# Optimization experiments

Hardware: AMD Instinct MI355X
Metric: run time of the kernel (lower is better)

Reference implementation:

```python
import jax, jax.numpy as jnp
import numpy as np

DIM = 1024
HEADS = 8
DIM_HEAD = 64
INNER = HEADS * DIM_HEAD  # 512


def setup_inputs() -> dict:
    key = jax.random.key(0)
    k1, k2, k3, k4 = jax.random.split(key, 4)
    x = jax.random.normal(k1, (4, 4096, DIM), dtype=jnp.float32)
    W_qkv = jax.random.normal(k2, (DIM, 3 * INNER), dtype=jnp.float32) * (DIM ** -0.5)
    W_out = jax.random.normal(k3, (INNER, DIM), dtype=jnp.float32) * (INNER ** -0.5)
    b_out = jax.random.normal(k4, (DIM,), dtype=jnp.float32) * 0.01
    return {"x": x, "W_qkv": W_qkv, "W_out": W_out, "b_out": b_out}


def reference(x, W_qkv, W_out, b_out):
    b, n, _ = x.shape
    qkv = x @ W_qkv                                   # [b, n, 3*inner]
    q, k, v = jnp.split(qkv, 3, axis=-1)              # each [b, n, inner]

    def to_heads(t):
        return t.reshape(b, n, HEADS, DIM_HEAD).transpose(0, 2, 1, 3)  # [b, h, n, d]

    q = jax.nn.elu(to_heads(q)) + 1.0
    k = jax.nn.elu(to_heads(k)) + 1.0
    v = to_heads(v)
    # kv summary matrix: [b, h, d, e]
    context = jnp.einsum('bhnd,bhne->bhde', k, v)
    out = jnp.einsum('bhde,bhnd->bhne', context, q)   # [b, h, n, e]
    out = out.transpose(0, 2, 1, 3).reshape(b, n, INNER)
    return out @ W_out + b_out
```

## Files before the change

### kernel.cpp

```cpp
#include <hip/hip_runtime.h>
#include <hip/hip_bf16.h>
#include <cstdint>

typedef __attribute__((ext_vector_type(4))) float f32x4;
typedef __attribute__((ext_vector_type(8))) short bf16x8;

__device__ __forceinline__ ushort f2bf(float f) {
  unsigned u = __builtin_bit_cast(unsigned, f);
  u += 0x7fffu + ((u >> 16) & 1u);
  return (ushort)(u >> 16);
}
__device__ __forceinline__ float bf2f(ushort h) {
  unsigned u = ((unsigned)h) << 16;
  return __builtin_bit_cast(float, u);
}

__device__ __forceinline__ void gload_lds16(const ushort* g, ushort* l) {
  __builtin_amdgcn_global_load_lds(
      (const __attribute__((address_space(1))) unsigned int*)g,
      (__attribute__((address_space(3))) unsigned int*)l, 16, 0, 0);
}

__device__ __forceinline__ void hard_barrier() {
  __builtin_amdgcn_sched_barrier(0);
  __builtin_amdgcn_s_barrier();
  __builtin_amdgcn_sched_barrier(0);
}

template <int N>
__device__ __forceinline__ void wait_vm() {
  if constexpr (N == 0) asm volatile("s_waitcnt vmcnt(0)" ::: "memory");
  else if constexpr (N == 4) asm volatile("s_waitcnt vmcnt(4)" ::: "memory");
  else static_assert(N < 0, "unsupported vmcnt");
}

__global__ __launch_bounds__(256) void cvt_x_kernel(const float4* __restrict__ x,
                                                    ushort4* __restrict__ xb, int n4) {
  int stride = gridDim.x * blockDim.x;
  for (int i = blockIdx.x * blockDim.x + threadIdx.x; i < n4; i += stride) {
    float4 f = x[i];
    ushort4 o;
    o.x = f2bf(f.x); o.y = f2bf(f.y); o.z = f2bf(f.z); o.w = f2bf(f.w);
    xb[i] = o;
  }
}

__global__ __launch_bounds__(256) void transpose_w_kernel(const float* __restrict__ W,
                                                          ushort* __restrict__ Wt) {
  __shared__ float tile[32][33];
  int n0 = blockIdx.x * 32;
  int k0 = blockIdx.y * 32;
  int tx = threadIdx.x;
  int ty = threadIdx.y;
  #pragma unroll
  for (int p = 0; p < 4; ++p) {
    int k = k0 + ty + p * 8;
    tile[ty + p * 8][tx] = W[(size_t)k * 1536 + n0 + tx];
  }
  __syncthreads();
  #pragma unroll
  for (int p = 0; p < 4; ++p) {
    int n = n0 + ty + p * 8;
    Wt[(size_t)n * 1024 + k0 + tx] = f2bf(tile[tx][ty + p * 8]);
  }
}

template <int LDA, int LDB, int NT>
__device__ __forceinline__ void gemm_core8(const ushort* __restrict__ A,
                                           const ushort* __restrict__ Bt,
                                           int row0, int col0, f32x4 acc[8][4],
                                           ushort* lds) {
  const int tid = threadIdx.x;
  const int l = tid & 63;
  const int wid = tid >> 6;
  const int fr = l & 15, fq = l >> 4;
  const int wr = wid >> 2, wc = wid & 3;

  const int srow = tid >> 2;
  const int lam = (tid & 3) ^ ((tid >> 3) & 3);
  const ushort* aG = A + (size_t)(row0 + srow) * LDA + lam * 8;
  const ushort* bG = Bt + (size_t)(col0 + srow) * LDB + lam * 8;

  auto stageA = [&](int tt, int kap) {
    ushort* d = lds + (tt & 1) * 32768 + kap * 8192 + tid * 8;
    const ushort* s = aG + tt * 64 + kap * 32;
    gload_lds16(s, d);
    gload_lds16(s + (size_t)128 * LDA, d + 4096);
  };
  auto stageB = [&](int tt, int kap) {
    ushort* d = lds + (tt & 1) * 32768 + 16384 + kap * 8192 + tid * 8;
    const ushort* s = bG + tt * 64 + kap * 32;
    gload_lds16(s, d);
    gload_lds16(s + (size_t)128 * LDB, d + 4096);
  };

  const int sig = fq ^ ((fr >> 1) & 3);
  const int aOff = wr * 4096 + fr * 32 + sig * 8;
  const int bOff = 16384 + wc * 2048 + fr * 32 + sig * 8;

  auto mfma16 = [&](const bf16x8 av[4], const bf16x8 bv[4], int mh) {
    __builtin_amdgcn_s_setprio(1);
    #pragma unroll
    for (int mm = 0; mm < 4; ++mm)
      #pragma unroll
      for (int n = 0; n < 4; ++n)
        acc[mh * 4 + mm][n] =
            __builtin_amdgcn_mfma_f32_16x16x32_bf16(av[mm], bv[n], acc[mh * 4 + mm][n], 0, 0, 0);
    __builtin_amdgcn_s_setprio(0);
  };

  stageA(0, 0); stageB(0, 0); stageA(0, 1); stageB(0, 1);
  wait_vm<4>();
  hard_barrier();

  for (int t = 0; t < NT; ++t) {
    const ushort* sb = lds + (t & 1) * 32768;
    const bool pre = (t + 1 < NT);
    bf16x8 av[4], bv[4];

    #pragma unroll
    for (int mm = 0; mm < 4; ++mm) av[mm] = *(const bf16x8*)(sb + aOff + mm * 512);
    #pragma unroll
    for (int n = 0; n < 4; ++n) bv[n] = *(const bf16x8*)(sb + bOff + n * 512);
    if (pre) stageA(t + 1, 0);
    hard_barrier();
    mfma16(av, bv, 0);

    #pragma unroll
    for (int mm = 0; mm < 4; ++mm) av[mm] = *(const bf16x8*)(sb + aOff + 2048 + mm * 512);
    if (pre) { stageB(t + 1, 0); wait_vm<4>(); } else { wait_vm<0>(); }
    hard_barrier();
    mfma16(av, bv, 1);

    #pragma unroll
    for (int mm = 0; mm < 4; ++mm) av[mm] = *(const bf16x8*)(sb + 8192 + aOff + mm * 512);
    #pragma unroll
    for (int n = 0; n < 4; ++n) bv[n] = *(const bf16x8*)(sb + 8192 + bOff + n * 512);
    if (pre) stageA(t + 1, 1);
    hard_barrier();
    mfma16(av, bv, 0);

    #pragma unroll
    for (int mm = 0; mm < 4; ++mm) av[mm] = *(const bf16x8*)(sb + 8192 + aOff + 2048 + mm * 512);
    if (pre) { stageB(t + 1, 1); wait_vm<4>(); }
    hard_barrier();
    mfma16(av, bv, 1);
  }
}

__device__ __forceinline__ void swz_grid(int nx, int& bx, int& by) {
  const int bid = blockIdx.x;
  const int nwg = gridDim.x;
  const int cpx = nwg >> 3;
  const int swz = (bid & 7) * cpx + (bid >> 3);
  by = swz / nx;
  bx = swz - by * nx;
}

__global__ __launch_bounds__(512, 1) void gemm_qkv_kernel(const ushort* __restrict__ xb,
                                                          const ushort* __restrict__ wt,
                                                          ushort* __restrict__ qkv) {
  __shared__ ushort lds[65536];
  f32x4 acc[8][4] = {};
  int bx, by;
  swz_grid(64, bx, by);
  const int row0 = bx * 256;
  const int col0 = by * 256;
  gemm_core8<1024, 1024, 16>(xb, wt, row0, col0, acc, lds);
  const int l = threadIdx.x & 63;
  const int wid = threadIdx.x >> 6;
  const int wr = wid >> 2, wc = wid & 3;
  const int fr = l & 15, fq = l >> 4;
  #pragma unroll
  for (int m = 0; m < 8; ++m) {
    #pragma unroll
    for (int n = 0; n < 4; ++n) {
      const int c = col0 + wc * 64 + n * 16 + fr;
      #pragma unroll
      for (int j = 0; j < 4; ++j) {
        const int r = row0 + wr * 128 + m * 16 + fq * 4 + j;
        float v = acc[m][n][j];
        if (c < 1024) v = (v > 0.f) ? (v + 1.f) : __expf(v);
        qkv[(size_t)r * 1536 + c] = f2bf(v);
      }
    }
  }
}

__global__ __launch_bounds__(256) void ctx_kernel(const ushort* __restrict__ qkv,
                                                  float* __restrict__ part) {
  const int bh = blockIdx.x;
  const int split = blockIdx.y;
  const int b = bh >> 3, h = bh & 7;
  const int t = threadIdx.x;
  const int d0 = (t >> 4) * 4;
  const int e0 = (t & 15) * 4;
  __shared__ ushort ks[64][64];
  __shared__ ushort vs[64][64];
  float acc[4][4] = {};
  const int rowBase = b * 4096 + split * 256;
  for (int chunk = 0; chunk < 256; chunk += 64) {
    __syncthreads();
    #pragma unroll
    for (int p = 0; p < 2; ++p) {
      const int r = (t >> 3) + p * 32;
      const int c = (t & 7) * 8;
      const ushort* src = qkv + (size_t)(rowBase + chunk + r) * 1536;
      *(uint4*)&ks[r][c] = *(const uint4*)(src + 512 + h * 64 + c);
      *(uint4*)&vs[r][c] = *(const uint4*)(src + 1024 + h * 64 + c);
    }
    __syncthreads();
    for (int r = 0; r < 64; ++r) {
      ushort4 ku = *(const ushort4*)&ks[r][d0];
      ushort4 vu = *(const ushort4*)&vs[r][e0];
      float kk[4] = {bf2f(ku.x), bf2f(ku.y), bf2f(ku.z), bf2f(ku.w)};
      float vv[4] = {bf2f(vu.x), bf2f(vu.y), bf2f(vu.z), bf2f(vu.w)};
      #pragma unroll
      for (int i = 0; i < 4; ++i)
        #pragma unroll
        for (int j = 0; j < 4; ++j)
          acc[i][j] += kk[i] * vv[j];
    }
  }
  float* dst = part + ((size_t)split * 32 + bh) * 4096;
  #pragma unroll
  for (int i = 0; i < 4; ++i)
    #pragma unroll
    for (int j = 0; j < 4; ++j)
      dst[(d0 + i) * 64 + (e0 + j)] = acc[i][j];
}

__global__ __launch_bounds__(256) void ctx_reduce_kernel(const float* __restrict__ part,
                                                         float* __restrict__ ctx) {
  const int i = blockIdx.x * 256 + threadIdx.x;
  float s = 0.f;
  #pragma unroll
  for (int sp = 0; sp < 16; ++sp) s += part[(size_t)sp * 131072 + i];
  ctx[i] = s;
}

__global__ __launch_bounds__(256) void weff_kernel(const float* __restrict__ ctx,
                                                   const float* __restrict__ Wout,
                                                   ushort* __restrict__ weff) {
  const int bh = blockIdx.x;
  const int h = bh & 7;
  const int m0 = blockIdx.y * 128;
  const int t = threadIdx.x;
  __shared__ float cs[64 * 64];
  __shared__ float ws[64][128];
  #pragma unroll
  for (int p = 0; p < 4; ++p) {
    const int idx = p * 1024 + t * 4;
    *(float4*)&cs[idx] = *(const float4*)&ctx[(size_t)bh * 4096 + idx];
  }
  #pragma unroll
  for (int p = 0; p < 8; ++p) {
    const int e = (t >> 5) + p * 8;
    const int c = (t & 31) * 4;
    *(float4*)&ws[e][c] = *(const float4*)&Wout[(size_t)(h * 64 + e) * 1024 + m0 + c];
  }
  __syncthreads();
  const int m = t & 127;
  const int dh = (t >> 7) * 32;
  float acc[32] = {};
  for (int e = 0; e < 64; ++e) {
    const float w = ws[e][m];
    #pragma unroll
    for (int i = 0; i < 32; ++i)
      acc[i] += cs[(dh + i) * 64 + e] * w;
  }
  ushort* dst = weff + ((size_t)(bh >> 3) * 1024 + m0 + m) * 512 + h * 64 + dh;
  #pragma unroll
  for (int i = 0; i < 32; ++i) dst[i] = f2bf(acc[i]);
}

__global__ __launch_bounds__(512, 1) void gemm_out_kernel(const ushort* __restrict__ qkv,
                                                          const ushort* __restrict__ weff,
                                                          const float* __restrict__ bout,
                                                          float* __restrict__ out) {
  __shared__ ushort lds[65536];
  f32x4 acc[8][4] = {};
  int bx, by;
  swz_grid(64, bx, by);
  const int row0 = bx * 256;
  const int col0 = by * 256;
  const int b = row0 >> 12;
  gemm_core8<1536, 512, 8>(qkv, weff + (size_t)b * 1024 * 512, row0, col0, acc, lds);
  const int l = threadIdx.x & 63;
  const int wid = threadIdx.x >> 6;
  const int wr = wid >> 2, wc = wid & 3;
  const int fr = l & 15, fq = l >> 4;
  #pragma unroll
  for (int m = 0; m < 8; ++m) {
    #pragma unroll
    for (int n = 0; n < 4; ++n) {
      const int c = col0 + wc * 64 + n * 16 + fr;
      const float bb = bout[c];
      #pragma unroll
      for (int j = 0; j < 4; ++j) {
        const int r = row0 + wr * 128 + m * 16 + fq * 4 + j;
        out[(size_t)r * 1024 + c] = acc[m][n][j] + bb;
      }
    }
  }
}

extern "C" void kernel_launch(void* const* d_in, const int* in_sizes, int n_in,
                              void* d_out, int out_size, void* d_ws, size_t ws_size,
                              hipStream_t stream) {
  const float* x    = (const float*)d_in[0];
  const float* Wqkv = (const float*)d_in[1];
  const float* Wout = (const float*)d_in[2];
  const float* bout = (const float*)d_in[3];
  float* out = (float*)d_out;
  char* ws = (char*)d_ws;

  ushort* xb   = (ushort*)(ws);
  ushort* wt   = (ushort*)(ws + 33554432);
  ushort* qkv  = (ushort*)(ws + 36700160);
  float*  part = (float* )(ws + 87031808);
  float*  ctx  = (float* )(ws + 95420416);
  ushort* weff = (ushort*)(ws + 95944704);

  cvt_x_kernel<<<2048, 256, 0, stream>>>((const float4*)x, (ushort4*)xb, 16384 * 1024 / 4);
  transpose_w_kernel<<<dim3(48, 32), dim3(32, 8), 0, stream>>>(Wqkv, wt);
  gemm_qkv_kernel<<<384, 512, 0, stream>>>(xb, wt, qkv);
  ctx_kernel<<<dim3(32, 16), 256, 0, stream>>>(qkv, part);
  ctx_reduce_kernel<<<512, 256, 0, stream>>>(part, ctx);
  weff_kernel<<<dim3(32, 8), 256, 0, stream>>>(ctx, Wout, weff);
  gemm_out_kernel<<<256, 512, 0, stream>>>(qkv, weff, bout, out);
}
```

Before: 155.9 us.

## Deepen GEMM LDS prefetch pipeline and drop XCD grid swizzle

Restructures the shared bf16 GEMM main loop so global-to-LDS loads are issued up to two K-steps ahead. Each half-tile is refilled as soon as its previous contents have been consumed, with an extra barrier after every MFMA block and a vmcnt(6) wait. This aims to hide more global-load latency behind the MFMAs. The blockIdx-based XCD swizzle is also replaced by a plain 2D grid, which may change L2 locality across chiplets, and the extra barriers add sync cost.

```diff
diff --git a/kernel.cpp b/kernel.cpp
--- a/kernel.cpp
+++ b/kernel.cpp
@@ -30,7 +30,7 @@
 template <int N>
 __device__ __forceinline__ void wait_vm() {
   if constexpr (N == 0) asm volatile("s_waitcnt vmcnt(0)" ::: "memory");
-  else if constexpr (N == 4) asm volatile("s_waitcnt vmcnt(4)" ::: "memory");
+  else if constexpr (N == 6) asm volatile("s_waitcnt vmcnt(6)" ::: "memory");
   else static_assert(N < 0, "unsupported vmcnt");
 }
 
@@ -66,10 +66,10 @@
 }
 
 template <int LDA, int LDB, int NT>
-__device__ __forceinline__ void gemm_core8(const ushort* __restrict__ A,
-                                           const ushort* __restrict__ Bt,
-                                           int row0, int col0, f32x4 acc[8][4],
-                                           ushort* lds) {
+__device__ __forceinline__ void gemm_core_m201(const ushort* __restrict__ A,
+                                               const ushort* __restrict__ Bt,
+                                               int row0, int col0, f32x4 acc[8][4],
+                                               ushort* lds) {
   const int tid = threadIdx.x;
   const int l = tid & 63;
   const int wid = tid >> 6;
@@ -109,52 +109,47 @@
     __builtin_amdgcn_s_setprio(0);
   };
 
-  stageA(0, 0); stageB(0, 0); stageA(0, 1); stageB(0, 1);
-  wait_vm<4>();
+  stageB(0, 0); stageA(0, 0); stageB(0, 1); stageA(0, 1);
+  stageB(1, 0); stageA(1, 0); stageB(1, 1);
+  wait_vm<6>();
   hard_barrier();
 
   for (int t = 0; t < NT; ++t) {
     const ushort* sb = lds + (t & 1) * 32768;
-    const bool pre = (t + 1 < NT);
     bf16x8 av[4], bv[4];
 
     #pragma unroll
     for (int mm = 0; mm < 4; ++mm) av[mm] = *(const bf16x8*)(sb + aOff + mm * 512);
     #pragma unroll
     for (int n = 0; n < 4; ++n) bv[n] = *(const bf16x8*)(sb + bOff + n * 512);
-    if (pre) stageA(t + 1, 0);
+    if (t + 1 < NT) stageA(t + 1, 1);
     hard_barrier();
     mfma16(av, bv, 0);
+    hard_barrier();
 
     #pragma unroll
     for (int mm = 0; mm < 4; ++mm) av[mm] = *(const bf16x8*)(sb + aOff + 2048 + mm * 512);
-    if (pre) { stageB(t + 1, 0); wait_vm<4>(); } else { wait_vm<0>(); }
+    if (t + 2 < NT) stageB(t + 2, 0);
     hard_barrier();
     mfma16(av, bv, 1);
+    hard_barrier();
 
     #pragma unroll
     for (int mm = 0; mm < 4; ++mm) av[mm] = *(const bf16x8*)(sb + 8192 + aOff + mm * 512);
     #pragma unroll
     for (int n = 0; n < 4; ++n) bv[n] = *(const bf16x8*)(sb + 8192 + bOff + n * 512);
-    if (pre) stageA(t + 1, 1);
+    if (t + 2 < NT) stageA(t + 2, 0);
     hard_barrier();
     mfma16(av, bv, 0);
+    hard_barrier();
 
     #pragma unroll
     for (int mm = 0; mm < 4; ++mm) av[mm] = *(const bf16x8*)(sb + 8192 + aOff + 2048 + mm * 512);
-    if (pre) { stageB(t + 1, 1); wait_vm<4>(); }
+    if (t + 2 < NT) { stageB(t + 2, 1); wait_vm<6>(); } else { wait_vm<0>(); }
     hard_barrier();
     mfma16(av, bv, 1);
-  }
-}
-
-__device__ __forceinline__ void swz_grid(int nx, int& bx, int& by) {
-  const int bid = blockIdx.x;
-  const int nwg = gridDim.x;
-  const int cpx = nwg >> 3;
-  const int swz = (bid & 7) * cpx + (bid >> 3);
-  by = swz / nx;
-  bx = swz - by * nx;
+    hard_barrier();
+  }
 }
 
 __global__ __launch_bounds__(512, 1) void gemm_qkv_kernel(const ushort* __restrict__ xb,
@@ -162,11 +157,9 @@
                                                           ushort* __restrict__ qkv) {
   __shared__ ushort lds[65536];
   f32x4 acc[8][4] = {};
-  int bx, by;
-  swz_grid(64, bx, by);
-  const int row0 = bx * 256;
-  const int col0 = by * 256;
-  gemm_core8<1024, 1024, 16>(xb, wt, row0, col0, acc, lds);
+  const int row0 = blockIdx.x * 256;
+  const int col0 = blockIdx.y * 256;
+  gemm_core_m201<1024, 1024, 16>(xb, wt, row0, col0, acc, lds);
   const int l = threadIdx.x & 63;
   const int wid = threadIdx.x >> 6;
   const int wr = wid >> 2, wc = wid & 3;
@@ -280,12 +273,10 @@
                                                           float* __restrict__ out) {
   __shared__ ushort lds[65536];
   f32x4 acc[8][4] = {};
-  int bx, by;
-  swz_grid(64, bx, by);
-  const int row0 = bx * 256;
-  const int col0 = by * 256;
+  const int row0 = blockIdx.x * 256;
+  const int col0 = blockIdx.y * 256;
   const int b = row0 >> 12;
-  gemm_core8<1536, 512, 8>(qkv, weff + (size_t)b * 1024 * 512, row0, col0, acc, lds);
+  gemm_core_m201<1536, 512, 8>(qkv, weff + (size_t)b * 1024 * 512, row0, col0, acc, lds);
   const int l = threadIdx.x & 63;
   const int wid = threadIdx.x >> 6;
   const int wr = wid >> 2, wc = wid & 3;
@@ -324,9 +315,9 @@
 
   cvt_x_kernel<<<2048, 256, 0, stream>>>((const float4*)x, (ushort4*)xb, 16384 * 1024 / 4);
   transpose_w_kernel<<<dim3(48, 32), dim3(32, 8), 0, stream>>>(Wqkv, wt);
-  gemm_qkv_kernel<<<384, 512, 0, stream>>>(xb, wt, qkv);
+  gemm_qkv_kernel<<<dim3(64, 6), 512, 0, stream>>>(xb, wt, qkv);
   ctx_kernel<<<dim3(32, 16), 256, 0, stream>>>(qkv, part);
   ctx_reduce_kernel<<<512, 256, 0, stream>>>(part, ctx);
   weff_kernel<<<dim3(32, 8), 256, 0, stream>>>(ctx, Wout, weff);
-  gemm_out_kernel<<<256, 512, 0, stream>>>(qkv, weff, bout, out);
-}
+  gemm_out_kernel<<<dim3(64, 4), 512, 0, stream>>>(qkv, weff, bout, out);
+}
```

After: 152.7 us. -2.1%, faster.
